# Performance work log

Hardware: AMD Instinct MI355X
Metric: run time of the kernel (lower is better)

## Reference

```python
import jax, jax.numpy as jnp
import numpy as np

B, C, T, H, W = 4, 256, 8, 28, 28
IC = 128  # inter_channels = in_channels // 2


def setup_inputs() -> dict:
    key = jax.random.key(0)
    ks = jax.random.split(key, 5)
    s_in = 1.0 / np.sqrt(C)
    s_ic = 1.0 / np.sqrt(IC)
    return {
        "x": jax.random.normal(ks[0], (B, C, T, H, W), dtype=jnp.float32),
        "Wg": jax.random.normal(ks[1], (IC, C), dtype=jnp.float32) * s_in,
        "Wtheta": jax.random.normal(ks[2], (IC, C), dtype=jnp.float32) * s_in,
        "Wphi": jax.random.normal(ks[3], (IC, C), dtype=jnp.float32) * s_in,
        "Wz": jax.random.normal(ks[4], (C, IC), dtype=jnp.float32) * s_ic,
    }


def reference(x, Wg, Wtheta, Wphi, Wz):
    b, c, t, h, w = x.shape
    n = t * h * w
    xf = x.reshape(b, c, n)  # 1x1x1 conv == channel GEMM over flattened positions
    g_x = jnp.einsum("oc,bcn->bon", Wg, xf)       # [B, IC, N]
    theta_x = jnp.einsum("oc,bcn->bon", Wtheta, xf)
    phi_x = jnp.einsum("oc,bcn->bon", Wphi, xf)
    # f = theta^T @ phi : [B, N, N]
    f = jnp.einsum("bcn,bcm->bnm", theta_x, phi_x)
    f_div_C = jax.nn.softmax(f, axis=-1)
    # y = f_div_C @ g^T : [B, N, IC] -> keep as [B, IC, N]
    y = jnp.einsum("bnm,bcm->bcn", f_div_C, g_x)  # [B, IC, N]
    z = jnp.einsum("oc,bcn->bon", Wz, y).reshape(b, c, t, h, w) + x
    return z
```

## Files before the change

kernel.cpp:

```cpp
#include <hip/hip_runtime.h>
#include <cstdint>


#define BB   4
#define CCH  256
#define NPOS 6272
#define ICH  128
#define BNIC ((size_t)BB * NPOS * ICH)
#define KSPL 4
#define KLEN (NPOS / KSPL)
#define TKF  32
#define NITK (KLEN / TKF)
#define SLACK 12.0f

typedef __attribute__((ext_vector_type(8)))  _Float16 h8v;
typedef __attribute__((ext_vector_type(16))) float fx16;

__device__ __forceinline__ unsigned short f2h(float f) {
  _Float16 h = (_Float16)f;
  return __builtin_bit_cast(unsigned short, h);
}
__device__ __forceinline__ unsigned int pkh(float lo, float hi) {
  return __builtin_bit_cast(unsigned int, __builtin_amdgcn_cvt_pkrtz(lo, hi));
}

__global__ __launch_bounds__(256, 1)
void wconv(const float* __restrict__ Wtheta, const float* __restrict__ Wphi,
           const float* __restrict__ Wg,
           unsigned short* __restrict__ Whi, unsigned short* __restrict__ Wlo) {
  const int idx4 = (blockIdx.x * 256 + threadIdx.x) * 4;
  const int p = idx4 >> 15;
  const float* W = (p == 0) ? Wtheta : (p == 1) ? Wphi : Wg;
  const float4 v = *(const float4*)&W[idx4 - (p << 15)];
  const float vv[4] = {v.x, v.y, v.z, v.w};
  ushort4 h, l;
  unsigned short* hp = (unsigned short*)&h;
  unsigned short* lp = (unsigned short*)&l;
  #pragma unroll
  for (int q = 0; q < 4; ++q) {
    _Float16 hh = (_Float16)vv[q];
    hp[q] = __builtin_bit_cast(unsigned short, hh);
    lp[q] = f2h(vv[q] - (float)hh);
  }
  *(ushort4*)&Whi[idx4] = h;
  *(ushort4*)&Wlo[idx4] = l;
}

__global__ __launch_bounds__(256, 2)
void proj_mfma(const float* __restrict__ x,
               const unsigned short* __restrict__ Whi,
               const unsigned short* __restrict__ Wlo,
               unsigned short* __restrict__ Qg,
               unsigned short* __restrict__ Kg,
               unsigned short* __restrict__ Vtg) {
  __shared__ unsigned short Xhi[32][24];
  __shared__ unsigned short Xlo[32][24];
  const int n0 = blockIdx.x * 32;
  const int b  = blockIdx.y;
  const int tid = threadIdx.x;
  const int lane = tid & 63, wv = tid >> 6;
  const int ln = lane & 31, g = lane >> 5;

  fx16 acc[3];
  acc[0] = (fx16)(0.0f); acc[1] = (fx16)(0.0f); acc[2] = (fx16)(0.0f);

  const int sn = tid & 31, cp = (tid >> 5) * 2;
  const float* xp = x + ((size_t)b * CCH + cp) * NPOS + n0 + sn;

  float pv0 = xp[0];
  float pv1 = xp[NPOS];

  for (int c0 = 0; c0 < CCH; c0 += 16) {
    {
      _Float16 h0 = (_Float16)pv0, h1 = (_Float16)pv1;
      ushort2 hh, ll;
      hh.x = __builtin_bit_cast(unsigned short, h0);
      hh.y = __builtin_bit_cast(unsigned short, h1);
      ll.x = f2h(pv0 - (float)h0);
      ll.y = f2h(pv1 - (float)h1);
      *(ushort2*)&Xhi[sn][cp] = hh;
      *(ushort2*)&Xlo[sn][cp] = ll;
    }
    if (c0 + 16 < CCH) {
      pv0 = xp[(size_t)(c0 + 16) * NPOS];
      pv1 = xp[(size_t)(c0 + 17) * NPOS];
    }
    __syncthreads();
    const h8v bxh = *(const h8v*)&Xhi[ln][g * 8];
    const h8v bxl = *(const h8v*)&Xlo[ln][g * 8];
    #pragma unroll
    for (int t = 0; t < 3; ++t) {
      const int T = wv * 3 + t;
      const size_t wb = ((size_t)(T * 32 + ln)) * CCH + c0 + g * 8;
      const h8v ah = *(const h8v*)&Whi[wb];
      const h8v al = *(const h8v*)&Wlo[wb];
      acc[t] = __builtin_amdgcn_mfma_f32_32x32x16_f16(ah, bxh, acc[t], 0, 0, 0);
      acc[t] = __builtin_amdgcn_mfma_f32_32x32x16_f16(ah, bxl, acc[t], 0, 0, 0);
      acc[t] = __builtin_amdgcn_mfma_f32_32x32x16_f16(al, bxh, acc[t], 0, 0, 0);
    }
    __syncthreads();
  }

  const float LOG2E = 1.4426950408889634f;
  const int n = n0 + ln;
  #pragma unroll
  for (int t = 0; t < 3; ++t) {
    const int T = wv * 3 + t;
    const int p = T >> 2;
    const int ot = (T & 3) * 32;
    if (p < 2) {
      unsigned short* Out = (p == 0) ? Qg : Kg;
      const float scl = (p == 0) ? LOG2E : 1.0f;
      #pragma unroll
      for (int q = 0; q < 4; ++q) {
        ushort4 v;
        v.x = f2h(acc[t][4 * q + 0] * scl);
        v.y = f2h(acc[t][4 * q + 1] * scl);
        v.z = f2h(acc[t][4 * q + 2] * scl);
        v.w = f2h(acc[t][4 * q + 3] * scl);
        *(ushort4*)&Out[((size_t)b * NPOS + n) * ICH + ot + 8 * q + 4 * g] = v;
      }
    } else {
      #pragma unroll
      for (int r = 0; r < 16; ++r) {
        const int o = ot + (r & 3) + 8 * (r >> 2) + 4 * g;
        Vtg[((size_t)b * ICH + o) * NPOS + n] = f2h(acc[t][r]);
      }
    }
  }
}

__global__ __launch_bounds__(256, 2)
void flash10(const unsigned short* __restrict__ Qg,
             const unsigned short* __restrict__ Kg,
             const unsigned short* __restrict__ Vtg,
             unsigned short* __restrict__ Opart,
             float* __restrict__ Mpart,
             float* __restrict__ Lpart) {
  __shared__ unsigned short Ks[2][TKF * 128];
  __shared__ unsigned short Vs[2][128 * 36];

  const int f   = blockIdx.x;
  const int xcd = f & 7, j = f >> 3;
  const int hi  = (j >= NITK) ? 1 : 0;
  const int slab = xcd * 2 + hi;
  const int itile = j - hi * NITK;
  const int b   = slab >> 2;
  const int spl = slab & 3;
  const int n0  = itile * 128;
  const int kb  = spl * KLEN;

  const int tid = threadIdx.x;
  const int lane = tid & 63, wv = tid >> 6;
  const int qlane = lane & 31, g = lane >> 5;
  const int swz = qlane & 15;

  h8v qf[8];
  {
    const size_t qbase = ((size_t)b * NPOS + n0 + 32 * wv + qlane) * ICH;
    #pragma unroll
    for (int cs = 0; cs < 8; ++cs)
      qf[cs] = *(const h8v*)&Qg[qbase + cs * 16 + g * 8];
  }

  {
    #pragma unroll
    for (int i = 0; i < 2; ++i) {
      const int kr = (tid >> 4) + i * 16, c = tid & 15;
      const uint4 v = *(const uint4*)&Kg[((size_t)b * NPOS + kb + kr) * ICH + c * 8];
      *(uint4*)&Ks[0][kr * 128 + (c ^ (kr & 15)) * 8] = v;
      const int idx = tid * 2 + i, dr = idx >> 2, cv = idx & 3;
      const uint4 w = *(const uint4*)&Vtg[((size_t)b * ICH + dr) * NPOS + kb + cv * 8];
      *(uint2*)&Vs[0][dr * 36 + cv * 8]     = make_uint2(w.x, w.y);
      *(uint2*)&Vs[0][dr * 36 + cv * 8 + 4] = make_uint2(w.z, w.w);
    }
  }
  __syncthreads();

  float m_run = -1e30f, m_true = -1e30f, l_run = 0.0f;
  fx16 accO[4];
  #pragma unroll
  for (int mt = 0; mt < 4; ++mt) accO[mt] = (fx16)(0.0f);

  uint4 stgK[2], stgV[2];

  for (int it = 0; it < NITK; ++it) {
    const int cur = it & 1;
    const bool pre = (it + 1 < NITK);
    if (pre) {
      const int k0n = kb + (it + 1) * TKF;
      #pragma unroll
      for (int i = 0; i < 2; ++i) {
        const int kr = (tid >> 4) + i * 16;
        stgK[i] = *(const uint4*)&Kg[((size_t)b * NPOS + k0n + kr) * ICH + (tid & 15) * 8];
        const int idx = tid * 2 + i, dr = idx >> 2, cv = idx & 3;
        stgV[i] = *(const uint4*)&Vtg[((size_t)b * ICH + dr) * NPOS + k0n + cv * 8];
      }
    }

    fx16 accS = (fx16)(0.0f);
    #pragma unroll
    for (int cs = 0; cs < 8; ++cs) {
      const h8v aK = *(const h8v*)&Ks[cur][qlane * 128 + ((2 * cs + g) ^ swz) * 8];
      accS = __builtin_amdgcn_mfma_f32_32x32x16_f16(aK, qf[cs], accS, 0, 0, 0);
    }

    float a0 = fmaxf(accS[0], accS[1]),   a1 = fmaxf(accS[2], accS[3]);
    float a2 = fmaxf(accS[4], accS[5]),   a3 = fmaxf(accS[6], accS[7]);
    float a4 = fmaxf(accS[8], accS[9]),   a5 = fmaxf(accS[10], accS[11]);
    float a6 = fmaxf(accS[12], accS[13]), a7 = fmaxf(accS[14], accS[15]);
    a0 = fmaxf(a0, a1); a2 = fmaxf(a2, a3); a4 = fmaxf(a4, a5); a6 = fmaxf(a6, a7);
    float mx = fmaxf(fmaxf(a0, a2), fmaxf(a4, a6));
    mx = fmaxf(mx, __shfl_xor(mx, 32));
    m_true = fmaxf(m_true, mx);
    const bool fold = __any(mx > m_run + SLACK);
    const float mn = fold ? fmaxf(m_run, mx) : m_run;
    float lsum = 0.0f;
    unsigned int pk[4][2];
    #pragma unroll
    for (int u = 0; u < 4; ++u) {
      const float p0 = exp2f(accS[4 * u + 0] - mn);
      const float p1 = exp2f(accS[4 * u + 1] - mn);
      const float p2 = exp2f(accS[4 * u + 2] - mn);
      const float p3 = exp2f(accS[4 * u + 3] - mn);
      lsum += (p0 + p1) + (p2 + p3);
      pk[u][0] = pkh(p0, p1);
      pk[u][1] = pkh(p2, p3);
    }
    lsum += __shfl_xor(lsum, 32);
    if (fold) {
      const float alpha = exp2f(m_run - mn);
      l_run = l_run * alpha + lsum;
      m_run = mn;
      #pragma unroll
      for (int mt = 0; mt < 4; ++mt)
        #pragma unroll
        for (int r = 0; r < 16; ++r) accO[mt][r] *= alpha;
    } else {
      l_run += lsum;
    }

    #pragma unroll
    for (int s = 0; s < 2; ++s) {
      const unsigned int s0 = pk[2 * s + (g ^ 1)][0];
      const unsigned int s1 = pk[2 * s + (g ^ 1)][1];
      const unsigned int t0 = __shfl_xor(s0, 32);
      const unsigned int t1 = __shfl_xor(s1, 32);
      union { unsigned int u[4]; h8v v; } bP;
      bP.u[0] = g ? t0 : pk[2 * s][0];
      bP.u[1] = g ? t1 : pk[2 * s][1];
      bP.u[2] = g ? pk[2 * s + 1][0] : t0;
      bP.u[3] = g ? pk[2 * s + 1][1] : t1;
      #pragma unroll
      for (int mt = 0; mt < 4; ++mt) {
        const int dr = 32 * mt + qlane;
        union { unsigned int u[4]; h8v v; } aV;
        const uint2 lo = *(const uint2*)&Vs[cur][dr * 36 + (2 * s + g) * 8];
        const uint2 hi = *(const uint2*)&Vs[cur][dr * 36 + (2 * s + g) * 8 + 4];
        aV.u[0] = lo.x; aV.u[1] = lo.y; aV.u[2] = hi.x; aV.u[3] = hi.y;
        accO[mt] = __builtin_amdgcn_mfma_f32_32x32x16_f16(aV.v, bP.v, accO[mt], 0, 0, 0);
      }
    }

    if (pre) {
      const int nb = cur ^ 1;
      #pragma unroll
      for (int i = 0; i < 2; ++i) {
        const int kr = (tid >> 4) + i * 16;
        *(uint4*)&Ks[nb][kr * 128 + ((tid & 15) ^ (kr & 15)) * 8] = stgK[i];
        const int idx = tid * 2 + i, dr = idx >> 2, cv = idx & 3;
        *(uint2*)&Vs[nb][dr * 36 + cv * 8]     = make_uint2(stgV[i].x, stgV[i].y);
        *(uint2*)&Vs[nb][dr * 36 + cv * 8 + 4] = make_uint2(stgV[i].z, stgV[i].w);
      }
    }
    __syncthreads();
  }

  const float scale = exp2f(m_run - m_true);
  const int ncol = n0 + 32 * wv + qlane;
  const size_t obase = (size_t)(b * KSPL + spl) * ICH * NPOS;
  #pragma unroll
  for (int mt = 0; mt < 4; ++mt)
    #pragma unroll
    for (int r = 0; r < 16; ++r) {
      const int d = 32 * mt + (r & 3) + 8 * (r >> 2) + 4 * g;
      Opart[obase + (size_t)d * NPOS + ncol] = f2h(accO[mt][r] * scale);
    }
  if (g == 0) {
    Mpart[(size_t)(b * KSPL + spl) * NPOS + ncol] = m_true;
    Lpart[(size_t)(b * KSPL + spl) * NPOS + ncol] = l_run * scale;
  }
}

__global__ __launch_bounds__(256, 2)
void merge_kernel(const unsigned short* __restrict__ Opart,
                  const float* __restrict__ Mpart,
                  const float* __restrict__ Lpart,
                  float* __restrict__ Yt) {
  const int idx = (blockIdx.x * 256 + threadIdx.x) * 2;
  const int d0  = blockIdx.y * 32;
  const int b = idx / NPOS, n = idx % NPOS;
  float m[KSPL][2], l[KSPL][2], M0 = -1e30f, M1 = -1e30f;
  #pragma unroll
  for (int s = 0; s < KSPL; ++s) {
    const size_t base = (size_t)(b * KSPL + s) * NPOS + n;
    m[s][0] = Mpart[base]; m[s][1] = Mpart[base + 1];
    l[s][0] = Lpart[base]; l[s][1] = Lpart[base + 1];
    M0 = fmaxf(M0, m[s][0]); M1 = fmaxf(M1, m[s][1]);
  }
  float w[KSPL][2], lt0 = 0.0f, lt1 = 0.0f;
  #pragma unroll
  for (int s = 0; s < KSPL; ++s) {
    w[s][0] = exp2f(m[s][0] - M0); lt0 += w[s][0] * l[s][0];
    w[s][1] = exp2f(m[s][1] - M1); lt1 += w[s][1] * l[s][1];
  }
  const float inv0 = 1.0f / lt0, inv1 = 1.0f / lt1;
  for (int d = d0; d < d0 + 32; ++d) {
    float a0 = 0.0f, a1 = 0.0f;
    #pragma unroll
    for (int s = 0; s < KSPL; ++s) {
      const unsigned int u = *(const unsigned int*)
        &Opart[((size_t)(b * KSPL + s) * ICH + d) * NPOS + n];
      a0 += w[s][0] * (float)__builtin_bit_cast(_Float16, (unsigned short)(u & 0xffff));
      a1 += w[s][1] * (float)__builtin_bit_cast(_Float16, (unsigned short)(u >> 16));
    }
    float2 o; o.x = a0 * inv0; o.y = a1 * inv1;
    *(float2*)&Yt[((size_t)b * ICH + d) * NPOS + n] = o;
  }
}

__global__ __launch_bounds__(256, 2)
void zres_kernel(const float* __restrict__ x,
                 const float* __restrict__ Wz,
                 const float* __restrict__ Yt,
                 float* __restrict__ out) {
  const int n0 = blockIdx.x * 128;
  const int c0 = blockIdx.y * 128;
  const int b  = blockIdx.z;
  __shared__ float Yts[16][128];
  __shared__ float Wzt[16][128];
  const int tid = threadIdx.x;
  const int lane = tid & 63, wv = tid >> 6;
  const int tn = lane & 7, tc = lane >> 3;
  const int nb = (wv & 1) * 64 + tn * 8;
  const int cb = (wv >> 1) * 64 + tc * 8;
  float acc[8][8] = {};

  for (int ic0 = 0; ic0 < ICH; ic0 += 16) {
    {
      const int nn = tid & 127, kh = tid >> 7;
      #pragma unroll
      for (int q = 0; q < 8; ++q) {
        const int kk = kh + q * 2;
        Yts[kk][nn] = Yt[((size_t)b * ICH + ic0 + kk) * NPOS + n0 + nn];
      }
      const int wk = tid & 15, wo = tid >> 4;
      #pragma unroll
      for (int q = 0; q < 8; ++q) {
        const int cc = wo + q * 16;
        Wzt[wk][cc] = Wz[(size_t)(c0 + cc) * ICH + ic0 + wk];
      }
    }
    __syncthreads();
    #pragma unroll
    for (int kk = 0; kk < 16; ++kk) {
      const float4 a0 = *(const float4*)&Wzt[kk][cb];
      const float4 a1 = *(const float4*)&Wzt[kk][cb + 4];
      const float4 b0 = *(const float4*)&Yts[kk][nb];
      const float4 b1 = *(const float4*)&Yts[kk][nb + 4];
      const float a_[8] = {a0.x, a0.y, a0.z, a0.w, a1.x, a1.y, a1.z, a1.w};
      const float b_[8] = {b0.x, b0.y, b0.z, b0.w, b1.x, b1.y, b1.z, b1.w};
      #pragma unroll
      for (int i = 0; i < 8; ++i)
        #pragma unroll
        for (int j = 0; j < 8; ++j) acc[i][j] += a_[i] * b_[j];
    }
    __syncthreads();
  }
  #pragma unroll
  for (int i = 0; i < 8; ++i) {
    const size_t base = ((size_t)(b * CCH + c0 + cb + i)) * NPOS + n0 + nb;
    const float4 x0 = *(const float4*)&x[base];
    const float4 x1 = *(const float4*)&x[base + 4];
    float4 v0, v1;
    v0.x = acc[i][0] + x0.x; v0.y = acc[i][1] + x0.y;
    v0.z = acc[i][2] + x0.z; v0.w = acc[i][3] + x0.w;
    v1.x = acc[i][4] + x1.x; v1.y = acc[i][5] + x1.y;
    v1.z = acc[i][6] + x1.z; v1.w = acc[i][7] + x1.w;
    *(float4*)&out[base]     = v0;
    *(float4*)&out[base + 4] = v1;
  }
}

extern "C" void kernel_launch(void* const* d_in, const int* in_sizes, int n_in,
                              void* d_out, int out_size, void* d_ws, size_t ws_size,
                              hipStream_t stream) {
  const float* x      = (const float*)d_in[0];
  const float* Wg     = (const float*)d_in[1];
  const float* Wtheta = (const float*)d_in[2];
  const float* Wphi   = (const float*)d_in[3];
  const float* Wz     = (const float*)d_in[4];
  float* out = (float*)d_out;

  unsigned short* Qg    = (unsigned short*)d_ws;
  unsigned short* Kg    = Qg + BNIC;
  unsigned short* Vtg   = Kg + BNIC;
  unsigned short* Opart = Vtg + BNIC;
  float* Mpart = (float*)(Opart + (size_t)KSPL * BNIC);
  float* Lpart = Mpart + (size_t)KSPL * BB * NPOS;
  float* Yt    = (float*)Qg;

  unsigned short* Whi = Opart;
  unsigned short* Wlo = Whi + 3 * 128 * 256;

  wconv<<<dim3(96), 256, 0, stream>>>(Wtheta, Wphi, Wg, Whi, Wlo);
  proj_mfma<<<dim3(NPOS / 32, BB), 256, 0, stream>>>(x, Whi, Wlo, Qg, Kg, Vtg);
  flash10 <<<dim3(BB * KSPL * NITK), 256, 0, stream>>>(Qg, Kg, Vtg, Opart, Mpart, Lpart);
  merge_kernel<<<dim3(BB * NPOS / 512, 4), 256, 0, stream>>>(Opart, Mpart, Lpart, Yt);
  zres_kernel<<<dim3(NPOS / 128, CCH / 128, BB), 256, 0, stream>>>(x, Wz, Yt, out);
}
```

Baseline: 342.1 us.

## Fuse split-K merge into output projection and use split-fp16 MFMA

```diff
diff --git a/kernel.cpp b/kernel.cpp
--- a/kernel.cpp
+++ b/kernel.cpp
@@ -22,6 +22,9 @@
 }
 __device__ __forceinline__ unsigned int pkh(float lo, float hi) {
   return __builtin_bit_cast(unsigned int, __builtin_amdgcn_cvt_pkrtz(lo, hi));
+}
+__device__ __forceinline__ float h2f(unsigned short u) {
+  return (float)__builtin_bit_cast(_Float16, u);
 }
 
 __global__ __launch_bounds__(256, 1)
@@ -293,103 +296,144 @@
 }
 
 __global__ __launch_bounds__(256, 2)
-void merge_kernel(const unsigned short* __restrict__ Opart,
-                  const float* __restrict__ Mpart,
-                  const float* __restrict__ Lpart,
-                  float* __restrict__ Yt) {
-  const int idx = (blockIdx.x * 256 + threadIdx.x) * 2;
-  const int d0  = blockIdx.y * 32;
-  const int b = idx / NPOS, n = idx % NPOS;
-  float m[KSPL][2], l[KSPL][2], M0 = -1e30f, M1 = -1e30f;
-  #pragma unroll
-  for (int s = 0; s < KSPL; ++s) {
-    const size_t base = (size_t)(b * KSPL + s) * NPOS + n;
-    m[s][0] = Mpart[base]; m[s][1] = Mpart[base + 1];
-    l[s][0] = Lpart[base]; l[s][1] = Lpart[base + 1];
-    M0 = fmaxf(M0, m[s][0]); M1 = fmaxf(M1, m[s][1]);
-  }
-  float w[KSPL][2], lt0 = 0.0f, lt1 = 0.0f;
-  #pragma unroll
-  for (int s = 0; s < KSPL; ++s) {
-    w[s][0] = exp2f(m[s][0] - M0); lt0 += w[s][0] * l[s][0];
-    w[s][1] = exp2f(m[s][1] - M1); lt1 += w[s][1] * l[s][1];
-  }
-  const float inv0 = 1.0f / lt0, inv1 = 1.0f / lt1;
-  for (int d = d0; d < d0 + 32; ++d) {
-    float a0 = 0.0f, a1 = 0.0f;
-    #pragma unroll
-    for (int s = 0; s < KSPL; ++s) {
-      const unsigned int u = *(const unsigned int*)
-        &Opart[((size_t)(b * KSPL + s) * ICH + d) * NPOS + n];
-      a0 += w[s][0] * (float)__builtin_bit_cast(_Float16, (unsigned short)(u & 0xffff));
-      a1 += w[s][1] * (float)__builtin_bit_cast(_Float16, (unsigned short)(u >> 16));
-    }
-    float2 o; o.x = a0 * inv0; o.y = a1 * inv1;
-    *(float2*)&Yt[((size_t)b * ICH + d) * NPOS + n] = o;
-  }
-}
-
-__global__ __launch_bounds__(256, 2)
-void zres_kernel(const float* __restrict__ x,
-                 const float* __restrict__ Wz,
-                 const float* __restrict__ Yt,
-                 float* __restrict__ out) {
+void mz_kernel(const float* __restrict__ x,
+               const float* __restrict__ Wz,
+               const unsigned short* __restrict__ Opart,
+               const float* __restrict__ Mpart,
+               const float* __restrict__ Lpart,
+               float* __restrict__ out) {
+  __shared__ float4 wgt[128];
+  __shared__ unsigned short Yh[128][24], Yl[128][24];
+  __shared__ unsigned short Wzh[128][24], Wzl[128][24];
+
   const int n0 = blockIdx.x * 128;
   const int c0 = blockIdx.y * 128;
   const int b  = blockIdx.z;
-  __shared__ float Yts[16][128];
-  __shared__ float Wzt[16][128];
   const int tid = threadIdx.x;
   const int lane = tid & 63, wv = tid >> 6;
-  const int tn = lane & 7, tc = lane >> 3;
-  const int nb = (wv & 1) * 64 + tn * 8;
-  const int cb = (wv >> 1) * 64 + tc * 8;
-  float acc[8][8] = {};
-
-  for (int ic0 = 0; ic0 < ICH; ic0 += 16) {
+  const int ln = lane & 31, g = lane >> 5;
+
+  if (tid < 128) {
+    const int n = n0 + tid;
+    float m[4], l[4];
+    #pragma unroll
+    for (int s = 0; s < 4; ++s) {
+      m[s] = Mpart[(size_t)(b * KSPL + s) * NPOS + n];
+      l[s] = Lpart[(size_t)(b * KSPL + s) * NPOS + n];
+    }
+    const float M0 = fmaxf(fmaxf(m[0], m[1]), fmaxf(m[2], m[3]));
+    float w[4], lt = 0.0f;
+    #pragma unroll
+    for (int s = 0; s < 4; ++s) { w[s] = exp2f(m[s] - M0); lt += w[s] * l[s]; }
+    const float inv = 1.0f / lt;
+    float4 o;
+    o.x = w[0] * inv; o.y = w[1] * inv; o.z = w[2] * inv; o.w = w[3] * inv;
+    wgt[tid] = o;
+  }
+  __syncthreads();
+
+  const int np  = tid & 63;
+  const int icg = tid >> 6;
+  const float4 wsA4 = wgt[2 * np];
+  const float4 wsB4 = wgt[2 * np + 1];
+  const float wA[4] = {wsA4.x, wsA4.y, wsA4.z, wsA4.w};
+  const float wB[4] = {wsB4.x, wsB4.y, wsB4.z, wsB4.w};
+  const int wc = tid >> 1, wh = (tid & 1) * 8;
+  const float* Wzrow = Wz + (size_t)(c0 + wc) * ICH + wh;
+  const int cpair = wv >> 1, npair = wv & 1;
+
+  fx16 acc[2][2];
+  acc[0][0] = (fx16)(0.0f); acc[0][1] = (fx16)(0.0f);
+  acc[1][0] = (fx16)(0.0f); acc[1][1] = (fx16)(0.0f);
+
+  for (int k0 = 0; k0 < ICH; k0 += 16) {
     {
-      const int nn = tid & 127, kh = tid >> 7;
-      #pragma unroll
-      for (int q = 0; q < 8; ++q) {
-        const int kk = kh + q * 2;
-        Yts[kk][nn] = Yt[((size_t)b * ICH + ic0 + kk) * NPOS + n0 + nn];
-      }
-      const int wk = tid & 15, wo = tid >> 4;
-      #pragma unroll
-      for (int q = 0; q < 8; ++q) {
-        const int cc = wo + q * 16;
-        Wzt[wk][cc] = Wz[(size_t)(c0 + cc) * ICH + ic0 + wk];
-      }
+      const float4 w0 = *(const float4*)&Wzrow[k0];
+      const float4 w1 = *(const float4*)&Wzrow[k0 + 4];
+      const float wv8[8] = {w0.x, w0.y, w0.z, w0.w, w1.x, w1.y, w1.z, w1.w};
+      unsigned int hu[4], lu[4];
+      #pragma unroll
+      for (int q = 0; q < 4; ++q) {
+        _Float16 h0 = (_Float16)wv8[2 * q], h1 = (_Float16)wv8[2 * q + 1];
+        hu[q] = (unsigned int)__builtin_bit_cast(unsigned short, h0) |
+                ((unsigned int)__builtin_bit_cast(unsigned short, h1) << 16);
+        lu[q] = (unsigned int)f2h(wv8[2 * q] - (float)h0) |
+                ((unsigned int)f2h(wv8[2 * q + 1] - (float)h1) << 16);
+      }
+      *(uint4*)&Wzh[wc][wh] = make_uint4(hu[0], hu[1], hu[2], hu[3]);
+      *(uint4*)&Wzl[wc][wh] = make_uint4(lu[0], lu[1], lu[2], lu[3]);
+    }
+    {
+      unsigned short h0a[4], h1a[4], l0a[4], l1a[4];
+      #pragma unroll
+      for (int j = 0; j < 4; ++j) {
+        const int ic = k0 + icg * 4 + j;
+        float y0 = 0.0f, y1 = 0.0f;
+        #pragma unroll
+        for (int s = 0; s < 4; ++s) {
+          const unsigned int u = *(const unsigned int*)
+            &Opart[((size_t)(b * KSPL + s) * ICH + ic) * NPOS + n0 + 2 * np];
+          y0 += wA[s] * h2f((unsigned short)(u & 0xffff));
+          y1 += wB[s] * h2f((unsigned short)(u >> 16));
+        }
+        _Float16 hh0 = (_Float16)y0, hh1 = (_Float16)y1;
+        h0a[j] = __builtin_bit_cast(unsigned short, hh0);
+        h1a[j] = __builtin_bit_cast(unsigned short, hh1);
+        l0a[j] = f2h(y0 - (float)hh0);
+        l1a[j] = f2h(y1 - (float)hh1);
+      }
+      const int kc = icg * 4;
+      *(uint2*)&Yh[2 * np][kc] = make_uint2(
+        (unsigned)h0a[0] | ((unsigned)h0a[1] << 16),
+        (unsigned)h0a[2] | ((unsigned)h0a[3] << 16));
+      *(uint2*)&Yh[2 * np + 1][kc] = make_uint2(
+        (unsigned)h1a[0] | ((unsigned)h1a[1] << 16),
+        (unsigned)h1a[2] | ((unsigned)h1a[3] << 16));
+      *(uint2*)&Yl[2 * np][kc] = make_uint2(
+        (unsigned)l0a[0] | ((unsigned)l0a[1] << 16),
+        (unsigned)l0a[2] | ((unsigned)l0a[3] << 16));
+      *(uint2*)&Yl[2 * np + 1][kc] = make_uint2(
+        (unsigned)l1a[0] | ((unsigned)l1a[1] << 16),
+        (unsigned)l1a[2] | ((unsigned)l1a[3] << 16));
     }
     __syncthreads();
-    #pragma unroll
-    for (int kk = 0; kk < 16; ++kk) {
-      const float4 a0 = *(const float4*)&Wzt[kk][cb];
-      const float4 a1 = *(const float4*)&Wzt[kk][cb + 4];
-      const float4 b0 = *(const float4*)&Yts[kk][nb];
-      const float4 b1 = *(const float4*)&Yts[kk][nb + 4];
-      const float a_[8] = {a0.x, a0.y, a0.z, a0.w, a1.x, a1.y, a1.z, a1.w};
-      const float b_[8] = {b0.x, b0.y, b0.z, b0.w, b1.x, b1.y, b1.z, b1.w};
-      #pragma unroll
-      for (int i = 0; i < 8; ++i)
-        #pragma unroll
-        for (int j = 0; j < 8; ++j) acc[i][j] += a_[i] * b_[j];
-    }
+
+    h8v Ah[2], Al[2], Bh[2], Bl[2];
+    #pragma unroll
+    for (int ci = 0; ci < 2; ++ci) {
+      const int cr = (cpair * 2 + ci) * 32 + ln;
+      Ah[ci] = *(const h8v*)&Wzh[cr][g * 8];
+      Al[ci] = *(const h8v*)&Wzl[cr][g * 8];
+    }
+    #pragma unroll
+    for (int ni = 0; ni < 2; ++ni) {
+      const int nr = (npair * 2 + ni) * 32 + ln;
+      Bh[ni] = *(const h8v*)&Yh[nr][g * 8];
+      Bl[ni] = *(const h8v*)&Yl[nr][g * 8];
+    }
+    #pragma unroll
+    for (int ci = 0; ci < 2; ++ci)
+      #pragma unroll
+      for (int ni = 0; ni < 2; ++ni) {
+        acc[ci][ni] = __builtin_amdgcn_mfma_f32_32x32x16_f16(Ah[ci], Bh[ni], acc[ci][ni], 0, 0, 0);
+        acc[ci][ni] = __builtin_amdgcn_mfma_f32_32x32x16_f16(Ah[ci], Bl[ni], acc[ci][ni], 0, 0, 0);
+        acc[ci][ni] = __builtin_amdgcn_mfma_f32_32x32x16_f16(Al[ci], Bh[ni], acc[ci][ni], 0, 0, 0);
+      }
     __syncthreads();
   }
+
   #pragma unroll
-  for (int i = 0; i < 8; ++i) {
-    const size_t base = ((size_t)(b * CCH + c0 + cb + i)) * NPOS + n0 + nb;
-    const float4 x0 = *(const float4*)&x[base];
-    const float4 x1 = *(const float4*)&x[base + 4];
-    float4 v0, v1;
-    v0.x = acc[i][0] + x0.x; v0.y = acc[i][1] + x0.y;
-    v0.z = acc[i][2] + x0.z; v0.w = acc[i][3] + x0.w;
-    v1.x = acc[i][4] + x1.x; v1.y = acc[i][5] + x1.y;
-    v1.z = acc[i][6] + x1.z; v1.w = acc[i][7] + x1.w;
-    *(float4*)&out[base]     = v0;
-    *(float4*)&out[base + 4] = v1;
-  }
+  for (int ci = 0; ci < 2; ++ci)
+    #pragma unroll
+    for (int ni = 0; ni < 2; ++ni) {
+      const int n = n0 + npair * 64 + ni * 32 + ln;
+      #pragma unroll
+      for (int r = 0; r < 16; ++r) {
+        const int c = c0 + cpair * 64 + ci * 32 + (r & 3) + 8 * (r >> 2) + 4 * g;
+        const size_t base = ((size_t)(b * CCH + c)) * NPOS + n;
+        out[base] = acc[ci][ni][r] + x[base];
+      }
+    }
 }
 
 extern "C" void kernel_launch(void* const* d_in, const int* in_sizes, int n_in,
@@ -408,7 +452,6 @@
   unsigned short* Opart = Vtg + BNIC;
   float* Mpart = (float*)(Opart + (size_t)KSPL * BNIC);
   float* Lpart = Mpart + (size_t)KSPL * BB * NPOS;
-  float* Yt    = (float*)Qg;
 
   unsigned short* Whi = Opart;
   unsigned short* Wlo = Whi + 3 * 128 * 256;
@@ -416,6 +459,5 @@
   wconv<<<dim3(96), 256, 0, stream>>>(Wtheta, Wphi, Wg, Whi, Wlo);
   proj_mfma<<<dim3(NPOS / 32, BB), 256, 0, stream>>>(x, Whi, Wlo, Qg, Kg, Vtg);
   flash10 <<<dim3(BB * KSPL * NITK), 256, 0, stream>>>(Qg, Kg, Vtg, Opart, Mpart, Lpart);
-  merge_kernel<<<dim3(BB * NPOS / 512, 4), 256, 0, stream>>>(Opart, Mpart, Lpart, Yt);
-  zres_kernel<<<dim3(NPOS / 128, CCH / 128, BB), 256, 0, stream>>>(x, Wz, Yt, out);
-}
+  mz_kernel<<<dim3(NPOS / 128, CCH / 128, BB), 256, 0, stream>>>(x, Wz, Opart, Mpart, Lpart, out);
+}
```

New measurement: 316.3 us. 1.08x faster.
